# Performance work log

Hardware: AMD Instinct MI355X
Metric: run time of the kernel (lower is better)

Reference implementation:

```python
import jax, jax.numpy as jnp
import numpy as np

B, T, D, H = 2, 2048, 1024, 16
DH = D // H


def setup_inputs() -> dict:
    key = jax.random.key(0)
    k1, k2, k3, k4 = jax.random.split(key, 4)
    x = jax.random.normal(k1, (B, T, D), dtype=jnp.float32)
    k = jax.random.normal(k2, (B, H, T, DH), dtype=jnp.float32)
    v = jax.random.normal(k3, (B, H, T, DH), dtype=jnp.float32)
    Wq = jax.random.normal(k4, (D, D), dtype=jnp.float32) * (1.0 / np.sqrt(D))
    return {"x": x, "k": k, "v": v, "Wq": Wq}


def reference(x, k, v, Wq):
    b, t, d = x.shape
    h = k.shape[1]
    scale = 1.0 / jnp.sqrt(jnp.float32(d))  # note: sqrt(d), NOT sqrt(d/h), per source
    # q = Linear(d, d, bias=False): y = x @ Wq.T, then split into heads
    q = jnp.einsum('btd,ed->bte', x, Wq).reshape(b, t, h, -1).transpose(0, 2, 1, 3)  # [b,h,t,dh]
    scores = jnp.einsum('bhqd,bhkd->bhqk', q, k) * scale  # [b,h,t,t]
    causal = jnp.triu(jnp.ones((t, t), dtype=bool), k=1)  # True above diagonal -> masked
    scores = jnp.where(causal[None, None], -jnp.inf, scores)
    a = jax.nn.softmax(scores, axis=-1)
    out = jnp.einsum('bhqk,bhkd->bhqd', a, v).transpose(0, 2, 1, 3).reshape(b, t, d)
    return x + out
```

## Files before the change

kernel.cpp:

```cpp
#include <hip/hip_runtime.h>
#include <hip/hip_bf16.h>

#define B_ 2
#define T_ 2048
#define D_ 1024
#define H_ 16
#define DH_ 64

typedef __attribute__((ext_vector_type(8))) short bf16x8;
typedef __attribute__((ext_vector_type(4))) short bf16x4;
typedef __attribute__((ext_vector_type(4))) float f32x4;
typedef __attribute__((ext_vector_type(8))) unsigned short u16x8;

__device__ __forceinline__ unsigned short f2bf(float f) {
    unsigned int u = __float_as_uint(f);
    return (unsigned short)((u + 0x7FFFu + ((u >> 16) & 1u)) >> 16);
}

__device__ __forceinline__ f32x4 mfma16(bf16x4 a, bf16x4 b, f32x4 c) {
#if defined(__HIP_DEVICE_COMPILE__)
    return __builtin_amdgcn_mfma_f32_16x16x16bf16_1k(a, b, c, 0, 0, 0);
#else
    return c;
#endif
}

__device__ __forceinline__ float fast_exp2(float x) {
#if defined(__HIP_DEVICE_COMPILE__)
    return __builtin_amdgcn_exp2f(x);
#else
    return exp2f(x);
#endif
}

__global__ __launch_bounds__(256) void conv_kernel(
    const float* __restrict__ k, const float* __restrict__ v,
    const float* __restrict__ x, const float* __restrict__ Wq,
    unsigned short* __restrict__ kb, unsigned short* __restrict__ vt,
    unsigned short* __restrict__ xb, unsigned short* __restrict__ wqb)
{
    __shared__ float Ts[64][65];
    const int tid = threadIdx.x;
    const int bi = blockIdx.x;

    if (bi < 1152) {
        const float* src;
        unsigned short* dst;
        if (bi < 512)       { src = k  + (size_t)bi * 8192;
                              dst = kb  + (size_t)bi * 8192; }
        else if (bi < 1024) { src = x  + (size_t)(bi - 512) * 8192;
                              dst = xb  + (size_t)(bi - 512) * 8192; }
        else                { src = Wq + (size_t)(bi - 1024) * 8192;
                              dst = wqb + (size_t)(bi - 1024) * 8192; }
        #pragma unroll
        for (int u = 0; u < 8; ++u) {
            const int o = u * 1024 + tid * 4;
            const float4 a = *(const float4*)(src + o);
            ushort4 s;
            s.x = f2bf(a.x); s.y = f2bf(a.y);
            s.z = f2bf(a.z); s.w = f2bf(a.w);
            *(ushort4*)(dst + o) = s;
        }
        return;
    }

    const int idx = bi - 1152;
    const int t0 = (idx & 31) * 64;
    const int hb = idx >> 5;
    const size_t bh = (size_t)(hb >> 4) * H_ + (hb & 15);
    #pragma unroll
    for (int u = 0; u < 4; ++u) {
        const int tr = u * 16 + (tid >> 4);
        const int dc = (tid & 15) * 4;
        const float4 r = *(const float4*)(v + (bh * T_ + t0 + tr) * DH_ + dc);
        Ts[tr][dc + 0] = r.x; Ts[tr][dc + 1] = r.y;
        Ts[tr][dc + 2] = r.z; Ts[tr][dc + 3] = r.w;
    }
    __syncthreads();
    #pragma unroll
    for (int u = 0; u < 4; ++u) {
        const int dh = u * 16 + (tid >> 4);
        const int tc = (tid & 15) * 4;
        ushort4 o;
        o.x = f2bf(Ts[tc + 0][dh]); o.y = f2bf(Ts[tc + 1][dh]);
        o.z = f2bf(Ts[tc + 2][dh]); o.w = f2bf(Ts[tc + 3][dh]);
        *(ushort4*)(vt + (bh * DH_ + dh) * T_ + t0 + tc) = o;
    }
}

__global__ __launch_bounds__(256, 4) void mega_attn(
    const unsigned short* __restrict__ xb,
    const unsigned short* __restrict__ wqb,
    const unsigned short* __restrict__ kb,
    const unsigned short* __restrict__ vt,
    const float* __restrict__ xg,
    float* __restrict__ out)
{
    __shared__ __align__(16) char lds_raw[36864];
    unsigned short (*Ws0)[72] = (unsigned short(*)[72])(lds_raw);
    unsigned short (*Xs0)[72] = (unsigned short(*)[72])(lds_raw + 9216);
    unsigned short (*Ws1)[72] = (unsigned short(*)[72])(lds_raw + 18432);
    unsigned short (*Xs1)[72] = (unsigned short(*)[72])(lds_raw + 27648);
    unsigned short (*Qs)[72]  = (unsigned short(*)[72])(lds_raw + 27648);
    unsigned short (*Ks0)[72] = (unsigned short(*)[72])(lds_raw);
    unsigned short (*Ks1)[72] = (unsigned short(*)[72])(lds_raw + 9216);
    unsigned short (*Vs0)[72] = (unsigned short(*)[72])(lds_raw + 18432);
    unsigned short (*Vs1)[72] = (unsigned short(*)[72])(lds_raw + 27648);

    const int tid = threadIdx.x;
    const int lane = tid & 63;
    const int w = tid >> 6;
    const int l15 = lane & 15, l4 = lane >> 4;
    const int bi = blockIdx.x;

    const int qt = 31 - (bi >> 5);
    const int hb = bi & 31;
    const int h = hb & 15, b = hb >> 4;
    const int q0 = qt * 64;
    const size_t bh = (size_t)b * H_ + h;

    const int srow = tid >> 2;
    const int scol = (tid & 3) * 16;

    f32x4 acc[4] = {};
    {
        const unsigned short* xg0 = xb  + ((size_t)b * T_ + q0 + srow) * D_ + scol;
        const unsigned short* wg0 = wqb + (size_t)(h * 64 + srow) * D_ + scol;

        uint4 xr0 = *(const uint4*)(xg0);
        uint4 xr1 = *(const uint4*)(xg0 + 8);
        uint4 wr0 = *(const uint4*)(wg0);
        uint4 wr1 = *(const uint4*)(wg0 + 8);
        *(uint4*)&Xs0[srow][scol] = xr0;
        *(uint4*)&Xs0[srow][scol + 8] = xr1;
        *(uint4*)&Ws0[srow][scol] = wr0;
        *(uint4*)&Ws0[srow][scol + 8] = wr1;
        __syncthreads();

        int p = 0;
        for (int it = 0; it < 16; ++it) {
            if (it < 15) {
                const int kk = (it + 1) * 64;
                xr0 = *(const uint4*)(xg0 + kk);
                xr1 = *(const uint4*)(xg0 + kk + 8);
                wr0 = *(const uint4*)(wg0 + kk);
                wr1 = *(const uint4*)(wg0 + kk + 8);
            }
            unsigned short (*Wp)[72] = p ? Ws1 : Ws0;
            unsigned short (*Xp)[72] = p ? Xs1 : Xs0;
            #pragma unroll
            for (int kc = 0; kc < 2; ++kc) {
                const bf16x8 wf = *(const bf16x8*)&Wp[w * 16 + l15][kc * 32 + l4 * 8];
                #pragma unroll
                for (int nt = 0; nt < 4; ++nt) {
                    const bf16x8 xf = *(const bf16x8*)&Xp[nt * 16 + l15][kc * 32 + l4 * 8];
                    acc[nt] = __builtin_amdgcn_mfma_f32_16x16x32_bf16(wf, xf, acc[nt], 0, 0, 0);
                }
            }
            if (it < 15) {
                unsigned short (*Wn)[72] = p ? Ws0 : Ws1;
                unsigned short (*Xn)[72] = p ? Xs0 : Xs1;
                *(uint4*)&Xn[srow][scol] = xr0;
                *(uint4*)&Xn[srow][scol + 8] = xr1;
                *(uint4*)&Wn[srow][scol] = wr0;
                *(uint4*)&Wn[srow][scol + 8] = wr1;
                __syncthreads();
                p ^= 1;
            }
        }
    }
    __syncthreads();

    {
        const float qscale = (1.0f / 32.0f) * 1.4426950408889634f;
        #pragma unroll
        for (int nt = 0; nt < 4; ++nt) {
            ushort4 o;
            o.x = f2bf(acc[nt][0] * qscale); o.y = f2bf(acc[nt][1] * qscale);
            o.z = f2bf(acc[nt][2] * qscale); o.w = f2bf(acc[nt][3] * qscale);
            *(ushort4*)&Qs[nt * 16 + l15][w * 16 + l4 * 4] = o;
        }
    }
    __syncthreads();

    bf16x8 qf[2];
    #pragma unroll
    for (int kc = 0; kc < 2; ++kc)
        qf[kc] = *(const bf16x8*)&Qs[w * 16 + l15][kc * 32 + l4 * 8];

    f32x4 o_acc[4] = {};
    float m_i = -INFINITY, l_i = 0.0f;

    {
        const unsigned short* gk = kb + (bh * T_ + srow) * DH_ + scol;
        *(uint4*)&Ks0[srow][scol] = *(const uint4*)gk;
        *(uint4*)&Ks0[srow][scol + 8] = *(const uint4*)(gk + 8);
        const unsigned short* gv = vt + (bh * DH_ + srow) * T_ + scol;
        *(uint4*)&Vs0[srow][scol] = *(const uint4*)gv;
        *(uint4*)&Vs0[srow][scol + 8] = *(const uint4*)(gv + 8);
    }
    __syncthreads();

    int p = 0;
    for (int j0 = 0; j0 <= q0; j0 += 64) {
        unsigned short (*Ksp)[72] = p ? Ks1 : Ks0;
        unsigned short (*Vsp)[72] = p ? Vs1 : Vs0;
        unsigned short (*Ksn)[72] = p ? Ks0 : Ks1;
        unsigned short (*Vsn)[72] = p ? Vs0 : Vs1;
        const bool more = (j0 < q0);

        const int jn = more ? j0 + 64 : 0;
        uint4 kr0, kr1, vr0, vr1;
        {
            const unsigned short* gk = kb + (bh * T_ + jn + srow) * DH_ + scol;
            kr0 = *(const uint4*)gk;
            kr1 = *(const uint4*)(gk + 8);
            const unsigned short* gv = vt + (bh * DH_ + srow) * T_ + jn + scol;
            vr0 = *(const uint4*)gv;
            vr1 = *(const uint4*)(gv + 8);
        }

        f32x4 st[4] = {};
        __builtin_amdgcn_s_setprio(1);
        #pragma unroll
        for (int kc = 0; kc < 2; ++kc) {
            #pragma unroll
            for (int nt = 0; nt < 4; ++nt) {
                const bf16x8 kf = *(const bf16x8*)&Ksp[nt * 16 + l15][kc * 32 + l4 * 8];
                st[nt] = __builtin_amdgcn_mfma_f32_16x16x32_bf16(kf, qf[kc], st[nt], 0, 0, 0);
            }
        }
        __builtin_amdgcn_s_setprio(0);

        if (j0 == q0) {
            const int thr = w * 16 + l15 - l4 * 4;
            #pragma unroll
            for (int nt = 0; nt < 4; ++nt)
                #pragma unroll
                for (int r = 0; r < 4; ++r)
                    if (nt * 16 + r > thr) st[nt][r] = -INFINITY;
        }

        float rm = -INFINITY;
        #pragma unroll
        for (int nt = 0; nt < 4; ++nt)
            #pragma unroll
            for (int r = 0; r < 4; ++r) rm = fmaxf(rm, st[nt][r]);
        rm = fmaxf(rm, __shfl_xor(rm, 16));
        rm = fmaxf(rm, __shfl_xor(rm, 32));

        if (__all(rm <= m_i)) {
            float rs = 0.0f;
            #pragma unroll
            for (int nt = 0; nt < 4; ++nt)
                #pragma unroll
                for (int r = 0; r < 4; ++r) {
                    const float pv = fast_exp2(st[nt][r] - m_i);
                    st[nt][r] = pv;
                    rs += pv;
                }
            rs += __shfl_xor(rs, 16);
            rs += __shfl_xor(rs, 32);
            l_i += rs;
        } else {
            const float mn = fmaxf(m_i, rm);
            const float alpha = fast_exp2(m_i - mn);
            float rs = 0.0f;
            #pragma unroll
            for (int nt = 0; nt < 4; ++nt)
                #pragma unroll
                for (int r = 0; r < 4; ++r) {
                    const float pv = fast_exp2(st[nt][r] - mn);
                    st[nt][r] = pv;
                    rs += pv;
                }
            rs += __shfl_xor(rs, 16);
            rs += __shfl_xor(rs, 32);
            l_i = l_i * alpha + rs;
            m_i = mn;
            #pragma unroll
            for (int mt = 0; mt < 4; ++mt)
                #pragma unroll
                for (int r = 0; r < 4; ++r) o_acc[mt][r] *= alpha;
        }

        bf16x4 pf[4];
        #pragma unroll
        for (int nt = 0; nt < 4; ++nt) {
            union { unsigned int u[2]; bf16x4 s; } cv;
            cv.u[0] = __builtin_amdgcn_perm(__float_as_uint(st[nt][1]),
                                            __float_as_uint(st[nt][0]), 0x07060302u);
            cv.u[1] = __builtin_amdgcn_perm(__float_as_uint(st[nt][3]),
                                            __float_as_uint(st[nt][2]), 0x07060302u);
            pf[nt] = cv.s;
        }

        __builtin_amdgcn_s_setprio(1);
        #pragma unroll
        for (int c = 0; c < 4; ++c) {
            #pragma unroll
            for (int mt = 0; mt < 4; ++mt) {
                const bf16x4 vf = *(const bf16x4*)&Vsp[mt * 16 + l15][c * 16 + l4 * 4];
                o_acc[mt] = mfma16(vf, pf[c], o_acc[mt]);
            }
        }
        __builtin_amdgcn_s_setprio(0);

        if (more) {
            *(uint4*)&Ksn[srow][scol] = kr0;
            *(uint4*)&Ksn[srow][scol + 8] = kr1;
            *(uint4*)&Vsn[srow][scol] = vr0;
            *(uint4*)&Vsn[srow][scol + 8] = vr1;
            __syncthreads();
            p ^= 1;
        }
    }

    const float inv = 1.0f / l_i;
    const int qrow = q0 + w * 16 + l15;
    #pragma unroll
    for (int mt = 0; mt < 4; ++mt) {
        #pragma unroll
        for (int r = 0; r < 4; ++r) {
            const int d = h * DH_ + mt * 16 + l4 * 4 + r;
            const size_t off = ((size_t)b * T_ + qrow) * D_ + d;
            out[off] = xg[off] + o_acc[mt][r] * inv;
        }
    }
}

extern "C" void kernel_launch(void* const* d_in, const int* in_sizes, int n_in,
                              void* d_out, int out_size, void* d_ws, size_t ws_size,
                              hipStream_t stream) {
    const float* x  = (const float*)d_in[0];
    const float* k  = (const float*)d_in[1];
    const float* v  = (const float*)d_in[2];
    const float* Wq = (const float*)d_in[3];
    float* out = (float*)d_out;

    const size_t NE = (size_t)B_ * H_ * T_ * DH_;
    unsigned short* kb  = (unsigned short*)d_ws;
    unsigned short* vt  = kb + NE;
    unsigned short* xb  = vt + NE;
    unsigned short* wqb = xb + NE;

    conv_kernel<<<2176, 256, 0, stream>>>(k, v, x, Wq, kb, vt, xb, wqb);
    mega_attn<<<1024, 256, 0, stream>>>(xb, wqb, kb, vt, x, out);
}
```

Measured before the change: 154.5 us.

## Load K/V fragments directly from global memory, removing LDS double buffering

The attention loop no longer stages K and V tiles through double-buffered shared memory with block barriers. Each wave instead reads its MFMA operand fragments for K and V straight from global memory into registers at the start of each iteration. This removes the LDS writes, LDS reads and __syncthreads per tile. In exchange, all four waves fetch the same K/V tile redundantly, the loads are uncoalesced and small, and there is no prefetch to hide their latency.

```diff
diff --git a/kernel.cpp b/kernel.cpp
--- a/kernel.cpp
+++ b/kernel.cpp
@@ -102,10 +102,6 @@
     unsigned short (*Ws1)[72] = (unsigned short(*)[72])(lds_raw + 18432);
     unsigned short (*Xs1)[72] = (unsigned short(*)[72])(lds_raw + 27648);
     unsigned short (*Qs)[72]  = (unsigned short(*)[72])(lds_raw + 27648);
-    unsigned short (*Ks0)[72] = (unsigned short(*)[72])(lds_raw);
-    unsigned short (*Ks1)[72] = (unsigned short(*)[72])(lds_raw + 9216);
-    unsigned short (*Vs0)[72] = (unsigned short(*)[72])(lds_raw + 18432);
-    unsigned short (*Vs1)[72] = (unsigned short(*)[72])(lds_raw + 27648);
 
     const int tid = threadIdx.x;
     const int lane = tid & 63;
@@ -191,44 +187,33 @@
     f32x4 o_acc[4] = {};
     float m_i = -INFINITY, l_i = 0.0f;
 
-    {
-        const unsigned short* gk = kb + (bh * T_ + srow) * DH_ + scol;
-        *(uint4*)&Ks0[srow][scol] = *(const uint4*)gk;
-        *(uint4*)&Ks0[srow][scol + 8] = *(const uint4*)(gk + 8);
-        const unsigned short* gv = vt + (bh * DH_ + srow) * T_ + scol;
-        *(uint4*)&Vs0[srow][scol] = *(const uint4*)gv;
-        *(uint4*)&Vs0[srow][scol + 8] = *(const uint4*)(gv + 8);
-    }
-    __syncthreads();
-
-    int p = 0;
+    const unsigned short* kbase = kb + bh * (size_t)T_ * DH_;
+    const unsigned short* vbase = vt + bh * (size_t)DH_ * T_;
+
     for (int j0 = 0; j0 <= q0; j0 += 64) {
-        unsigned short (*Ksp)[72] = p ? Ks1 : Ks0;
-        unsigned short (*Vsp)[72] = p ? Vs1 : Vs0;
-        unsigned short (*Ksn)[72] = p ? Ks0 : Ks1;
-        unsigned short (*Vsn)[72] = p ? Vs0 : Vs1;
-        const bool more = (j0 < q0);
-
-        const int jn = more ? j0 + 64 : 0;
-        uint4 kr0, kr1, vr0, vr1;
-        {
-            const unsigned short* gk = kb + (bh * T_ + jn + srow) * DH_ + scol;
-            kr0 = *(const uint4*)gk;
-            kr1 = *(const uint4*)(gk + 8);
-            const unsigned short* gv = vt + (bh * DH_ + srow) * T_ + jn + scol;
-            vr0 = *(const uint4*)gv;
-            vr1 = *(const uint4*)(gv + 8);
-        }
+        bf16x8 kf[2][4];
+        #pragma unroll
+        for (int kc = 0; kc < 2; ++kc)
+            #pragma unroll
+            for (int nt = 0; nt < 4; ++nt)
+                kf[kc][nt] = *(const bf16x8*)(
+                    kbase + (size_t)(j0 + nt * 16 + l15) * DH_ + kc * 32 + l4 * 8);
+
+        bf16x4 vf[4][4];
+        #pragma unroll
+        for (int c = 0; c < 4; ++c)
+            #pragma unroll
+            for (int mt = 0; mt < 4; ++mt)
+                vf[c][mt] = *(const bf16x4*)(
+                    vbase + (size_t)(mt * 16 + l15) * T_ + j0 + c * 16 + l4 * 4);
 
         f32x4 st[4] = {};
         __builtin_amdgcn_s_setprio(1);
         #pragma unroll
         for (int kc = 0; kc < 2; ++kc) {
             #pragma unroll
-            for (int nt = 0; nt < 4; ++nt) {
-                const bf16x8 kf = *(const bf16x8*)&Ksp[nt * 16 + l15][kc * 32 + l4 * 8];
-                st[nt] = __builtin_amdgcn_mfma_f32_16x16x32_bf16(kf, qf[kc], st[nt], 0, 0, 0);
-            }
+            for (int nt = 0; nt < 4; ++nt)
+                st[nt] = __builtin_amdgcn_mfma_f32_16x16x32_bf16(kf[kc][nt], qf[kc], st[nt], 0, 0, 0);
         }
         __builtin_amdgcn_s_setprio(0);
 
@@ -299,21 +284,10 @@
         #pragma unroll
         for (int c = 0; c < 4; ++c) {
             #pragma unroll
-            for (int mt = 0; mt < 4; ++mt) {
-                const bf16x4 vf = *(const bf16x4*)&Vsp[mt * 16 + l15][c * 16 + l4 * 4];
-                o_acc[mt] = mfma16(vf, pf[c], o_acc[mt]);
-            }
+            for (int mt = 0; mt < 4; ++mt)
+                o_acc[mt] = mfma16(vf[c][mt], pf[c], o_acc[mt]);
         }
         __builtin_amdgcn_s_setprio(0);
-
-        if (more) {
-            *(uint4*)&Ksn[srow][scol] = kr0;
-            *(uint4*)&Ksn[srow][scol + 8] = kr1;
-            *(uint4*)&Vsn[srow][scol] = vr0;
-            *(uint4*)&Vsn[srow][scol + 8] = vr1;
-            __syncthreads();
-            p ^= 1;
-        }
     }
 
     const float inv = 1.0f / l_i;
```

Measured after the change: 321.4 us. 2.08x slower.

## Split KV loop across two wave groups per block with LDS softmax merge

Applied to the files above, without the earlier changes.

Doubles the block to 512 threads. Two groups of four waves each take alternating 64-key tiles of the causal range, and their partial max, sum and output are merged through LDS at the end. The Q projection still runs only on the first four waves, while all threads share the global-to-LDS loads. This is meant to halve the serial KV loop length per block and raise wave-level parallelism. The cost is extra barriers, idle waves during the projection and the merge, and the launch bound asking for 8 blocks of 512 threads, which puts more pressure on registers.

```diff
diff --git a/kernel.cpp b/kernel.cpp
--- a/kernel.cpp
+++ b/kernel.cpp
@@ -88,7 +88,7 @@
     }
 }
 
-__global__ __launch_bounds__(256, 4) void mega_attn(
+__global__ __launch_bounds__(512, 8) void mega_attn(
     const unsigned short* __restrict__ xb,
     const unsigned short* __restrict__ wqb,
     const unsigned short* __restrict__ kb,
@@ -110,6 +110,8 @@
     const int tid = threadIdx.x;
     const int lane = tid & 63;
     const int w = tid >> 6;
+    const int wl = w & 3;
+    const int g = w >> 2;
     const int l15 = lane & 15, l4 = lane >> 4;
     const int bi = blockIdx.x;
 
@@ -119,51 +121,45 @@
     const int q0 = qt * 64;
     const size_t bh = (size_t)b * H_ + h;
 
-    const int srow = tid >> 2;
-    const int scol = (tid & 3) * 16;
+    const int srow = tid >> 3;
+    const int scol = (tid & 7) * 8;
 
     f32x4 acc[4] = {};
     {
         const unsigned short* xg0 = xb  + ((size_t)b * T_ + q0 + srow) * D_ + scol;
         const unsigned short* wg0 = wqb + (size_t)(h * 64 + srow) * D_ + scol;
 
-        uint4 xr0 = *(const uint4*)(xg0);
-        uint4 xr1 = *(const uint4*)(xg0 + 8);
-        uint4 wr0 = *(const uint4*)(wg0);
-        uint4 wr1 = *(const uint4*)(wg0 + 8);
-        *(uint4*)&Xs0[srow][scol] = xr0;
-        *(uint4*)&Xs0[srow][scol + 8] = xr1;
-        *(uint4*)&Ws0[srow][scol] = wr0;
-        *(uint4*)&Ws0[srow][scol + 8] = wr1;
+        uint4 xr = *(const uint4*)(xg0);
+        uint4 wr = *(const uint4*)(wg0);
+        *(uint4*)&Xs0[srow][scol] = xr;
+        *(uint4*)&Ws0[srow][scol] = wr;
         __syncthreads();
 
         int p = 0;
         for (int it = 0; it < 16; ++it) {
             if (it < 15) {
                 const int kk = (it + 1) * 64;
-                xr0 = *(const uint4*)(xg0 + kk);
-                xr1 = *(const uint4*)(xg0 + kk + 8);
-                wr0 = *(const uint4*)(wg0 + kk);
-                wr1 = *(const uint4*)(wg0 + kk + 8);
-            }
-            unsigned short (*Wp)[72] = p ? Ws1 : Ws0;
-            unsigned short (*Xp)[72] = p ? Xs1 : Xs0;
-            #pragma unroll
-            for (int kc = 0; kc < 2; ++kc) {
-                const bf16x8 wf = *(const bf16x8*)&Wp[w * 16 + l15][kc * 32 + l4 * 8];
-                #pragma unroll
-                for (int nt = 0; nt < 4; ++nt) {
-                    const bf16x8 xf = *(const bf16x8*)&Xp[nt * 16 + l15][kc * 32 + l4 * 8];
-                    acc[nt] = __builtin_amdgcn_mfma_f32_16x16x32_bf16(wf, xf, acc[nt], 0, 0, 0);
+                xr = *(const uint4*)(xg0 + kk);
+                wr = *(const uint4*)(wg0 + kk);
+            }
+            if (w < 4) {
+                unsigned short (*Wp)[72] = p ? Ws1 : Ws0;
+                unsigned short (*Xp)[72] = p ? Xs1 : Xs0;
+                #pragma unroll
+                for (int kc = 0; kc < 2; ++kc) {
+                    const bf16x8 wf = *(const bf16x8*)&Wp[w * 16 + l15][kc * 32 + l4 * 8];
+                    #pragma unroll
+                    for (int nt = 0; nt < 4; ++nt) {
+                        const bf16x8 xf = *(const bf16x8*)&Xp[nt * 16 + l15][kc * 32 + l4 * 8];
+                        acc[nt] = __builtin_amdgcn_mfma_f32_16x16x32_bf16(wf, xf, acc[nt], 0, 0, 0);
+                    }
                 }
             }
             if (it < 15) {
                 unsigned short (*Wn)[72] = p ? Ws0 : Ws1;
                 unsigned short (*Xn)[72] = p ? Xs0 : Xs1;
-                *(uint4*)&Xn[srow][scol] = xr0;
-                *(uint4*)&Xn[srow][scol + 8] = xr1;
-                *(uint4*)&Wn[srow][scol] = wr0;
-                *(uint4*)&Wn[srow][scol + 8] = wr1;
+                *(uint4*)&Xn[srow][scol] = xr;
+                *(uint4*)&Wn[srow][scol] = wr;
                 __syncthreads();
                 p ^= 1;
             }
@@ -171,7 +167,7 @@
     }
     __syncthreads();
 
-    {
+    if (w < 4) {
         const float qscale = (1.0f / 32.0f) * 1.4426950408889634f;
         #pragma unroll
         for (int nt = 0; nt < 4; ++nt) {
@@ -186,145 +182,165 @@
     bf16x8 qf[2];
     #pragma unroll
     for (int kc = 0; kc < 2; ++kc)
-        qf[kc] = *(const bf16x8*)&Qs[w * 16 + l15][kc * 32 + l4 * 8];
+        qf[kc] = *(const bf16x8*)&Qs[wl * 16 + l15][kc * 32 + l4 * 8];
+
+    __syncthreads();
 
     f32x4 o_acc[4] = {};
     float m_i = -INFINITY, l_i = 0.0f;
 
     {
-        const unsigned short* gk = kb + (bh * T_ + srow) * DH_ + scol;
-        *(uint4*)&Ks0[srow][scol] = *(const uint4*)gk;
-        *(uint4*)&Ks0[srow][scol + 8] = *(const uint4*)(gk + 8);
-        const unsigned short* gv = vt + (bh * DH_ + srow) * T_ + scol;
-        *(uint4*)&Vs0[srow][scol] = *(const uint4*)gv;
-        *(uint4*)&Vs0[srow][scol + 8] = *(const uint4*)(gv + 8);
-    }
-    __syncthreads();
-
-    int p = 0;
-    for (int j0 = 0; j0 <= q0; j0 += 64) {
-        unsigned short (*Ksp)[72] = p ? Ks1 : Ks0;
-        unsigned short (*Vsp)[72] = p ? Vs1 : Vs0;
-        unsigned short (*Ksn)[72] = p ? Ks0 : Ks1;
-        unsigned short (*Vsn)[72] = p ? Vs0 : Vs1;
-        const bool more = (j0 < q0);
-
-        const int jn = more ? j0 + 64 : 0;
-        uint4 kr0, kr1, vr0, vr1;
-        {
-            const unsigned short* gk = kb + (bh * T_ + jn + srow) * DH_ + scol;
-            kr0 = *(const uint4*)gk;
-            kr1 = *(const uint4*)(gk + 8);
-            const unsigned short* gv = vt + (bh * DH_ + srow) * T_ + jn + scol;
-            vr0 = *(const uint4*)gv;
-            vr1 = *(const uint4*)(gv + 8);
-        }
-
-        f32x4 st[4] = {};
-        __builtin_amdgcn_s_setprio(1);
+        const int j1 = (q0 >= 64) ? 64 : 0;
+        *(uint4*)&Ks0[srow][scol] = *(const uint4*)(kb + (bh * T_ + srow) * DH_ + scol);
+        *(uint4*)&Ks1[srow][scol] = *(const uint4*)(kb + (bh * T_ + j1 + srow) * DH_ + scol);
+        *(uint4*)&Vs0[srow][scol] = *(const uint4*)(vt + (bh * DH_ + srow) * T_ + scol);
+        *(uint4*)&Vs1[srow][scol] = *(const uint4*)(vt + (bh * DH_ + srow) * T_ + j1 + scol);
+    }
+    __syncthreads();
+
+    unsigned short (*Ksp)[72] = g ? Ks1 : Ks0;
+    unsigned short (*Vsp)[72] = g ? Vs1 : Vs0;
+    const int thr = wl * 16 + l15 - l4 * 4;
+    const int nsup = (qt + 2) >> 1;
+
+    for (int s = 0; s < nsup; ++s) {
+        const bool more = (s + 1 < nsup);
+
+        const int jnA = more ? (2 * s + 2) * 64 : 0;
+        const int jnB = ((2 * s + 3) * 64 <= q0) ? (2 * s + 3) * 64 : 0;
+        uint4 pkA = *(const uint4*)(kb + (bh * T_ + jnA + srow) * DH_ + scol);
+        uint4 pkB = *(const uint4*)(kb + (bh * T_ + jnB + srow) * DH_ + scol);
+        uint4 pvA = *(const uint4*)(vt + (bh * DH_ + srow) * T_ + jnA + scol);
+        uint4 pvB = *(const uint4*)(vt + (bh * DH_ + srow) * T_ + jnB + scol);
+
+        const int myT = 2 * s + g;
+        if (myT <= qt) {
+            f32x4 st[4] = {};
+            __builtin_amdgcn_s_setprio(1);
+            #pragma unroll
+            for (int kc = 0; kc < 2; ++kc) {
+                #pragma unroll
+                for (int nt = 0; nt < 4; ++nt) {
+                    const bf16x8 kf = *(const bf16x8*)&Ksp[nt * 16 + l15][kc * 32 + l4 * 8];
+                    st[nt] = __builtin_amdgcn_mfma_f32_16x16x32_bf16(kf, qf[kc], st[nt], 0, 0, 0);
+                }
+            }
+            __builtin_amdgcn_s_setprio(0);
+
+            if (myT == qt) {
+                #pragma unroll
+                for (int nt = 0; nt < 4; ++nt)
+                    #pragma unroll
+                    for (int r = 0; r < 4; ++r)
+                        if (nt * 16 + r > thr) st[nt][r] = -INFINITY;
+            }
+
+            float rm = -INFINITY;
+            #pragma unroll
+            for (int nt = 0; nt < 4; ++nt)
+                #pragma unroll
+                for (int r = 0; r < 4; ++r) rm = fmaxf(rm, st[nt][r]);
+            rm = fmaxf(rm, __shfl_xor(rm, 16));
+            rm = fmaxf(rm, __shfl_xor(rm, 32));
+
+            if (__all(rm <= m_i)) {
+                float rs = 0.0f;
+                #pragma unroll
+                for (int nt = 0; nt < 4; ++nt)
+                    #pragma unroll
+                    for (int r = 0; r < 4; ++r) {
+                        const float pv = fast_exp2(st[nt][r] - m_i);
+                        st[nt][r] = pv;
+                        rs += pv;
+                    }
+                rs += __shfl_xor(rs, 16);
+                rs += __shfl_xor(rs, 32);
+                l_i += rs;
+            } else {
+                const float mn = fmaxf(m_i, rm);
+                const float alpha = fast_exp2(m_i - mn);
+                float rs = 0.0f;
+                #pragma unroll
+                for (int nt = 0; nt < 4; ++nt)
+                    #pragma unroll
+                    for (int r = 0; r < 4; ++r) {
+                        const float pv = fast_exp2(st[nt][r] - mn);
+                        st[nt][r] = pv;
+                        rs += pv;
+                    }
+                rs += __shfl_xor(rs, 16);
+                rs += __shfl_xor(rs, 32);
+                l_i = l_i * alpha + rs;
+                m_i = mn;
+                #pragma unroll
+                for (int mt = 0; mt < 4; ++mt)
+                    #pragma unroll
+                    for (int r = 0; r < 4; ++r) o_acc[mt][r] *= alpha;
+            }
+
+            bf16x4 pf[4];
+            #pragma unroll
+            for (int nt = 0; nt < 4; ++nt) {
+                union { unsigned int u[2]; bf16x4 s2; } cv;
+                cv.u[0] = __builtin_amdgcn_perm(__float_as_uint(st[nt][1]),
+                                                __float_as_uint(st[nt][0]), 0x07060302u);
+                cv.u[1] = __builtin_amdgcn_perm(__float_as_uint(st[nt][3]),
+                                                __float_as_uint(st[nt][2]), 0x07060302u);
+                pf[nt] = cv.s2;
+            }
+
+            __builtin_amdgcn_s_setprio(1);
+            #pragma unroll
+            for (int c = 0; c < 4; ++c) {
+                #pragma unroll
+                for (int mt = 0; mt < 4; ++mt) {
+                    const bf16x4 vf = *(const bf16x4*)&Vsp[mt * 16 + l15][c * 16 + l4 * 4];
+                    o_acc[mt] = mfma16(vf, pf[c], o_acc[mt]);
+                }
+            }
+            __builtin_amdgcn_s_setprio(0);
+        }
+
+        if (more) {
+            __syncthreads();
+            *(uint4*)&Ks0[srow][scol] = pkA;
+            *(uint4*)&Ks1[srow][scol] = pkB;
+            *(uint4*)&Vs0[srow][scol] = pvA;
+            *(uint4*)&Vs1[srow][scol] = pvB;
+            __syncthreads();
+        }
+    }
+
+    __syncthreads();
+    float* mergeO  = (float*)lds_raw;
+    float* mergeML = (float*)(lds_raw + 18432);
+    if (g == 1) {
         #pragma unroll
-        for (int kc = 0; kc < 2; ++kc) {
-            #pragma unroll
-            for (int nt = 0; nt < 4; ++nt) {
-                const bf16x8 kf = *(const bf16x8*)&Ksp[nt * 16 + l15][kc * 32 + l4 * 8];
-                st[nt] = __builtin_amdgcn_mfma_f32_16x16x32_bf16(kf, qf[kc], st[nt], 0, 0, 0);
-            }
-        }
-        __builtin_amdgcn_s_setprio(0);
-
-        if (j0 == q0) {
-            const int thr = w * 16 + l15 - l4 * 4;
-            #pragma unroll
-            for (int nt = 0; nt < 4; ++nt)
-                #pragma unroll
-                for (int r = 0; r < 4; ++r)
-                    if (nt * 16 + r > thr) st[nt][r] = -INFINITY;
-        }
-
-        float rm = -INFINITY;
+        for (int mt = 0; mt < 4; ++mt)
+            *(f32x4*)&mergeO[(wl * 16 + l15) * 64 + mt * 16 + l4 * 4] = o_acc[mt];
+        if (l4 == 0) {
+            mergeML[(wl * 16 + l15) * 2]     = m_i;
+            mergeML[(wl * 16 + l15) * 2 + 1] = l_i;
+        }
+    }
+    __syncthreads();
+    if (g == 0) {
+        const float mBv = mergeML[(wl * 16 + l15) * 2];
+        const float lBv = mergeML[(wl * 16 + l15) * 2 + 1];
+        const float mF = fmaxf(m_i, mBv);
+        const float aA = fast_exp2(m_i - mF);
+        const float aB = fast_exp2(mBv - mF);
+        const float inv = 1.0f / (l_i * aA + lBv * aB);
+        const int qrow = q0 + wl * 16 + l15;
         #pragma unroll
-        for (int nt = 0; nt < 4; ++nt)
-            #pragma unroll
-            for (int r = 0; r < 4; ++r) rm = fmaxf(rm, st[nt][r]);
-        rm = fmaxf(rm, __shfl_xor(rm, 16));
-        rm = fmaxf(rm, __shfl_xor(rm, 32));
-
-        if (__all(rm <= m_i)) {
-            float rs = 0.0f;
-            #pragma unroll
-            for (int nt = 0; nt < 4; ++nt)
-                #pragma unroll
-                for (int r = 0; r < 4; ++r) {
-                    const float pv = fast_exp2(st[nt][r] - m_i);
-                    st[nt][r] = pv;
-                    rs += pv;
-                }
-            rs += __shfl_xor(rs, 16);
-            rs += __shfl_xor(rs, 32);
-            l_i += rs;
-        } else {
-            const float mn = fmaxf(m_i, rm);
-            const float alpha = fast_exp2(m_i - mn);
-            float rs = 0.0f;
-            #pragma unroll
-            for (int nt = 0; nt < 4; ++nt)
-                #pragma unroll
-                for (int r = 0; r < 4; ++r) {
-                    const float pv = fast_exp2(st[nt][r] - mn);
-                    st[nt][r] = pv;
-                    rs += pv;
-                }
-            rs += __shfl_xor(rs, 16);
-            rs += __shfl_xor(rs, 32);
-            l_i = l_i * alpha + rs;
-            m_i = mn;
-            #pragma unroll
-            for (int mt = 0; mt < 4; ++mt)
-                #pragma unroll
-                for (int r = 0; r < 4; ++r) o_acc[mt][r] *= alpha;
-        }
-
-        bf16x4 pf[4];
-        #pragma unroll
-        for (int nt = 0; nt < 4; ++nt) {
-            union { unsigned int u[2]; bf16x4 s; } cv;
-            cv.u[0] = __builtin_amdgcn_perm(__float_as_uint(st[nt][1]),
-                                            __float_as_uint(st[nt][0]), 0x07060302u);
-            cv.u[1] = __builtin_amdgcn_perm(__float_as_uint(st[nt][3]),
-                                            __float_as_uint(st[nt][2]), 0x07060302u);
-            pf[nt] = cv.s;
-        }
-
-        __builtin_amdgcn_s_setprio(1);
-        #pragma unroll
-        for (int c = 0; c < 4; ++c) {
-            #pragma unroll
-            for (int mt = 0; mt < 4; ++mt) {
-                const bf16x4 vf = *(const bf16x4*)&Vsp[mt * 16 + l15][c * 16 + l4 * 4];
-                o_acc[mt] = mfma16(vf, pf[c], o_acc[mt]);
-            }
-        }
-        __builtin_amdgcn_s_setprio(0);
-
-        if (more) {
-            *(uint4*)&Ksn[srow][scol] = kr0;
-            *(uint4*)&Ksn[srow][scol + 8] = kr1;
-            *(uint4*)&Vsn[srow][scol] = vr0;
-            *(uint4*)&Vsn[srow][scol + 8] = vr1;
-            __syncthreads();
-            p ^= 1;
-        }
-    }
-
-    const float inv = 1.0f / l_i;
-    const int qrow = q0 + w * 16 + l15;
-    #pragma unroll
-    for (int mt = 0; mt < 4; ++mt) {
-        #pragma unroll
-        for (int r = 0; r < 4; ++r) {
-            const int d = h * DH_ + mt * 16 + l4 * 4 + r;
-            const size_t off = ((size_t)b * T_ + qrow) * D_ + d;
-            out[off] = xg[off] + o_acc[mt][r] * inv;
+        for (int mt = 0; mt < 4; ++mt) {
+            #pragma unroll
+            for (int r = 0; r < 4; ++r) {
+                const float ob = mergeO[(wl * 16 + l15) * 64 + mt * 16 + l4 * 4 + r];
+                const int d = h * DH_ + mt * 16 + l4 * 4 + r;
+                const size_t off = ((size_t)b * T_ + qrow) * D_ + d;
+                out[off] = xg[off] + (o_acc[mt][r] * aA + ob * aB) * inv;
+            }
         }
     }
 }
@@ -345,5 +361,5 @@
     unsigned short* wqb = xb + NE;
 
     conv_kernel<<<2176, 256, 0, stream>>>(k, v, x, Wq, kb, vt, xb, wqb);
-    mega_attn<<<1024, 256, 0, stream>>>(xb, wqb, kb, vt, x, out);
-}
+    mega_attn<<<1024, 512, 0, stream>>>(xb, wqb, kb, vt, x, out);
+}
```

Result: slower. 330.1 us (+113.6%).
